# Performance work log

Measured on AMD Instinct MI355X. Metric: run time of the kernel, lower is better.

Reference implementation:

```python
import jax, jax.numpy as jnp
import numpy as np

THETA = 10000.0
NUM_HEADS = 16


def _rope(x, positions):
    # x: [B, H, S, Dk] (fp32), positions: [B, S] int
    d_k = x.shape[-1]
    k = jnp.arange(0, d_k, 2, dtype=jnp.float32)
    freqs = THETA ** (-k / d_k)                      # [Dk/2]
    angles = positions[..., None].astype(jnp.float32) * freqs  # [B, S, Dk/2]
    cos = jnp.cos(angles)[:, None, :, :]             # [B, 1, S, Dk/2]
    sin = jnp.sin(angles)[:, None, :, :]
    xr = x.reshape(*x.shape[:-1], d_k // 2, 2)
    x_even, x_odd = xr[..., 0], xr[..., 1]
    rot_even = x_even * cos - x_odd * sin
    rot_odd = x_even * sin + x_odd * cos
    out = jnp.stack([rot_even, rot_odd], axis=-1)
    return out.reshape(x.shape)


def setup_inputs() -> dict:
    key = jax.random.key(0)
    ks = jax.random.split(key, 6)
    B, S, D = 2, 2048, 1024
    std = (2.0 / (D + D)) ** 0.5
    x = jax.random.normal(ks[0], (B, S, D), dtype=jnp.float32)
    Wq = jax.random.normal(ks[1], (D, D), dtype=jnp.float32) * std
    Wk = jax.random.normal(ks[2], (D, D), dtype=jnp.float32) * std
    Wv = jax.random.normal(ks[3], (D, D), dtype=jnp.float32) * std
    Wo = jax.random.normal(ks[4], (D, D), dtype=jnp.float32) * std
    token_positions = jnp.broadcast_to(jnp.arange(S, dtype=jnp.int32), (B, S))
    return {"x": x, "Wq": Wq, "Wk": Wk, "Wv": Wv, "Wo": Wo,
            "token_positions": token_positions}


def reference(x, Wq, Wk, Wv, Wo, token_positions):
    B, S, D = x.shape
    H = NUM_HEADS
    Dk = D // H
    # QKV projections (no bias): y = x @ W.T
    def proj(W):
        return (x @ W.T).reshape(B, S, H, Dk).transpose(0, 2, 1, 3)  # [B,H,S,Dk]
    Q, K, V = proj(Wq), proj(Wk), proj(Wv)
    Q = _rope(Q, token_positions)
    K = _rope(K, token_positions)
    scale = 1.0 / jnp.sqrt(jnp.float32(Dk))
    scores = jnp.einsum('bhqd,bhkd->bhqk', Q, K) * scale  # [B,H,S,S]
    causal = jnp.tril(jnp.ones((S, S), dtype=bool))
    scores = jnp.where(causal, scores, -jnp.inf)
    attn = jax.nn.softmax(scores.astype(jnp.float32), axis=-1)
    out = jnp.einsum('bhqk,bhkd->bhqd', attn, V)          # [B,H,S,Dk]
    out = out.transpose(0, 2, 1, 3).reshape(B, S, D)
    return out @ Wo.T
```

## Files before the change

kernel.cpp:

```cpp
#include <hip/hip_runtime.h>
#include <math.h>

#define D_MODEL 1024
#define NHEADS 16
#define DK 64
#define SEQ 2048
#define BATCH 2
#define MROWS (BATCH * SEQ)

typedef __attribute__((ext_vector_type(8))) short bfrag8;
typedef __attribute__((ext_vector_type(4))) float f32x4;
typedef unsigned short u16;
typedef __attribute__((ext_vector_type(8))) u16 u16x8;
typedef __attribute__((ext_vector_type(4))) u16 u16x4;

#define GLOBAL_AS(p) ((const __attribute__((address_space(1))) void*)(p))
#define LDS_AS(p)    ((__attribute__((address_space(3))) void*)(p))

#define RAW_BARRIER()  __asm__ volatile("s_barrier" ::: "memory")
#define WAIT_VM4()     __asm__ volatile("s_waitcnt vmcnt(4)" ::: "memory")
#define WAIT_VM0()     __asm__ volatile("s_waitcnt vmcnt(0)" ::: "memory")

__device__ inline u16 f2bf(float f) {
  union { float f; unsigned u; } c; c.f = f;
  unsigned r = c.u + 0x7FFF + ((c.u >> 16) & 1);
  return (u16)(r >> 16);
}

__device__ inline unsigned pack_bf2(float lo, float hi) {
  return __builtin_amdgcn_perm(__float_as_uint(hi), __float_as_uint(lo), 0x07060302);
}

struct CvtPtrs { const float* src[5]; };

__global__ __launch_bounds__(256)
void convert_and_tab(CvtPtrs p, u16* __restrict__ dst,
                     const int* __restrict__ pos, float2* __restrict__ tab) {
  const int bi = blockIdx.x;
  if (bi < 8192) {
    size_t base = ((size_t)bi * 256 + threadIdx.x) * 4;
    const size_t XSZ = (size_t)MROWS * D_MODEL;
    const float* s; size_t off;
    if (base < XSZ) { s = p.src[0]; off = base; }
    else {
      size_t j = base - XSZ;
      s = p.src[1 + (int)(j >> 20)];
      off = j & ((1u << 20) - 1);
    }
    float4 v = *(const float4*)(s + off);
    u16 o[4] = { f2bf(v.x), f2bf(v.y), f2bf(v.z), f2bf(v.w) };
    *(u16x4*)(dst + base) = *(u16x4*)o;
  } else {
    int idx = (bi - 8192) * 256 + threadIdx.x;
    int i = idx & 31, bs = idx >> 5;
    float pp = (float)pos[bs];
    float freq = expf(-(float)i * 0.2878231366242558f);
    float sn, cs;
    sincosf(pp * freq, &sn, &cs);
    tab[idx] = make_float2(cs, sn);
  }
}

__device__ inline void gemm_core(const u16* __restrict__ A, const u16* __restrict__ B,
                                 int m0, int n0, u16* As, u16* Bs,
                                 f32x4 acc[4][4]) {
  const int tid = threadIdx.x;
  const int w = tid >> 6, lane = tid & 63;
  const int l15 = lane & 15, quad = lane >> 4;
  const int wm = w >> 1, wn = w & 1;
  const int srow = tid >> 2;
  const int scol = (tid & 3) * 8;

  #pragma unroll
  for (int mi = 0; mi < 4; ++mi)
    #pragma unroll
    for (int ni = 0; ni < 4; ++ni) acc[mi][ni] = (f32x4)0.f;

  for (int k0 = 0; k0 < D_MODEL; k0 += 32) {
    __syncthreads();
    #pragma unroll
    for (int i = 0; i < 2; ++i) {
      const u16* ga = A + (size_t)((i * 64 + srow) + m0) * D_MODEL + k0 + scol;
      const u16* gb = B + (size_t)((i * 64 + srow) + n0) * D_MODEL + k0 + scol;
      __builtin_amdgcn_global_load_lds(GLOBAL_AS(ga), LDS_AS(&As[(i * 64 + w * 16) * 32]), 16, 0, 0);
      __builtin_amdgcn_global_load_lds(GLOBAL_AS(gb), LDS_AS(&Bs[(i * 64 + w * 16) * 32]), 16, 0, 0);
    }
    __syncthreads();

    bfrag8 af[4], bfr[4];
    #pragma unroll
    for (int i = 0; i < 4; ++i) {
      af[i]  = *(const bfrag8*)&As[(wm * 64 + i * 16 + l15) * 32 + quad * 8];
      bfr[i] = *(const bfrag8*)&Bs[(wn * 64 + i * 16 + l15) * 32 + quad * 8];
    }
    #pragma unroll
    for (int mi = 0; mi < 4; ++mi)
      #pragma unroll
      for (int ni = 0; ni < 4; ++ni)
        acc[mi][ni] = __builtin_amdgcn_mfma_f32_16x16x32_bf16(af[mi], bfr[ni], acc[mi][ni], 0, 0, 0);
  }
}

struct QKVArgs { const u16* A[3]; const u16* B[3]; u16* dst[3]; const float2* tab; };

__global__ __launch_bounds__(256)
void gemm_qkv_fused(QKVArgs p) {
  __shared__ u16 As[128 * 32];
  __shared__ u16 Bs[128 * 32];
  const int z = blockIdx.z;
  const int bi = blockIdx.x;
  int m0, n0;
  if (z < 2) { m0 = (bi & 7) * 128; n0 = (bi >> 3) * 128; }
  else       { m0 = (bi >> 3) * 128; n0 = (bi & 7) * 128; }
  f32x4 acc[4][4];
  gemm_core(p.A[z], p.B[z], m0, n0, As, Bs, acc);

  const int tid = threadIdx.x;
  const int w = tid >> 6, lane = tid & 63;
  const int l15 = lane & 15, quad = lane >> 4;
  const int wm = w >> 1, wn = w & 1;
  u16* dst = p.dst[z];

  if (z < 2) {
    const int head = (m0 + wm * 64) >> 6;
    const float scale = (z == 0) ? 0.125f * 1.4426950408889634f : 1.0f;
    #pragma unroll
    for (int ni = 0; ni < 4; ++ni) {
      int sg = n0 + wn * 64 + ni * 16 + l15;
      int b = sg >> 11;
      int s = sg & (SEQ - 1);
      size_t ho = ((size_t)(b * NHEADS + head)) * SEQ * DK;
      #pragma unroll
      for (int mi = 0; mi < 4; ++mi) {
        float4 t = *(const float4*)&p.tab[(size_t)sg * 32 + mi * 8 + quad * 2];
        float e0 = acc[mi][ni][0], o0 = acc[mi][ni][1];
        float e1 = acc[mi][ni][2], o1 = acc[mi][ni][3];
        u16x4 ov = { f2bf((e0 * t.x - o0 * t.y) * scale),
                     f2bf((e0 * t.y + o0 * t.x) * scale),
                     f2bf((e1 * t.z - o1 * t.w) * scale),
                     f2bf((e1 * t.w + o1 * t.z) * scale) };
        *(u16x4*)&dst[ho + (size_t)s * DK + mi * 16 + quad * 4] = ov;
      }
    }
  } else {
    const int b = m0 >> 11;
    const int head = (n0 >> 6) + wn;
    const size_t ho = ((size_t)(b * NHEADS + head)) * SEQ * DK;
    const int row_base = m0 + wm * 64;
    #pragma unroll
    for (int mi = 0; mi < 4; ++mi)
      #pragma unroll
      for (int ni = 0; ni < 4; ++ni) {
        int d = ni * 16 + l15;
        int sb = (row_base + mi * 16 + quad * 4) & (SEQ - 1);
        u16 o[4];
        #pragma unroll
        for (int r = 0; r < 4; ++r) o[r] = f2bf(acc[mi][ni][r]);
        *(u16x4*)&dst[ho + (size_t)d * SEQ + sb] = *(u16x4*)o;
      }
  }
}

__global__ __launch_bounds__(256)
void gemm_out_bf16(const u16* __restrict__ A, const u16* __restrict__ B,
                   float* __restrict__ C) {
  __shared__ u16 As[128 * 32];
  __shared__ u16 Bs[64 * 32];
  const int m0 = blockIdx.y * 128, n0 = blockIdx.x * 64;
  const int tid = threadIdx.x;
  const int w = tid >> 6, lane = tid & 63;
  const int l15 = lane & 15, quad = lane >> 4;
  const int wm = w >> 1, wn = w & 1;
  const int lrow = lane >> 2;
  const int lcol = (lane & 3) * 8;

  f32x4 acc[4][2];
  #pragma unroll
  for (int mi = 0; mi < 4; ++mi)
    #pragma unroll
    for (int ni = 0; ni < 2; ++ni) acc[mi][ni] = (f32x4)0.f;

  for (int k0 = 0; k0 < D_MODEL; k0 += 32) {
    __syncthreads();
    #pragma unroll
    for (int i = 0; i < 2; ++i) {
      int row = (i * 4 + w) * 16 + lrow;
      const u16* ga = A + (size_t)(m0 + row) * D_MODEL + k0 + lcol;
      __builtin_amdgcn_global_load_lds(GLOBAL_AS(ga), LDS_AS(&As[(i * 4 + w) * 16 * 32]), 16, 0, 0);
    }
    {
      int row = w * 16 + lrow;
      const u16* gb = B + (size_t)(n0 + row) * D_MODEL + k0 + lcol;
      __builtin_amdgcn_global_load_lds(GLOBAL_AS(gb), LDS_AS(&Bs[w * 16 * 32]), 16, 0, 0);
    }
    __syncthreads();

    bfrag8 af[4], bfr[2];
    #pragma unroll
    for (int i = 0; i < 4; ++i)
      af[i] = *(const bfrag8*)&As[(wm * 64 + i * 16 + l15) * 32 + quad * 8];
    #pragma unroll
    for (int i = 0; i < 2; ++i)
      bfr[i] = *(const bfrag8*)&Bs[(wn * 32 + i * 16 + l15) * 32 + quad * 8];
    #pragma unroll
    for (int mi = 0; mi < 4; ++mi)
      #pragma unroll
      for (int ni = 0; ni < 2; ++ni)
        acc[mi][ni] = __builtin_amdgcn_mfma_f32_16x16x32_bf16(af[mi], bfr[ni], acc[mi][ni], 0, 0, 0);
  }

  #pragma unroll
  for (int mi = 0; mi < 4; ++mi)
    #pragma unroll
    for (int ni = 0; ni < 2; ++ni)
      #pragma unroll
      for (int r = 0; r < 4; ++r) {
        int row = m0 + wm * 64 + mi * 16 + quad * 4 + r;
        int col = n0 + wn * 32 + ni * 16 + l15;
        C[(size_t)row * D_MODEL + col] = acc[mi][ni][r];
      }
}

__global__ __launch_bounds__(256, 4)
void attn_mfma(const u16* __restrict__ Qbf, const u16* __restrict__ Kbf,
               const u16* __restrict__ Vtb, u16* __restrict__ obb) {
  __shared__ u16 Ks[2][64 * 64];
  __shared__ u16 Vt[2][64 * 64];

  const int tid = threadIdx.x;
  const int w = tid >> 6, lane = tid & 63;
  const int l15 = lane & 15, quad = lane >> 4;

  const int bid = blockIdx.x;
  const int hb = bid & 31;
  const int g  = bid >> 5;
  const int tt = (g & 7) | ((g & 16) >> 1);
  const int qt = (g & 8) ? (31 - tt) : tt;
  const int b = hb >> 4, h = hb & 15;
  const size_t ho = (size_t)hb * SEQ * DK;
  const int qrow_base = qt * 64 + w * 16;

  bfrag8 qf[2];
  #pragma unroll
  for (int hh = 0; hh < 2; ++hh)
    qf[hh] = *(const bfrag8*)&Qbf[ho + (size_t)(qrow_base + l15) * DK + hh * 32 + quad * 8];

  f32x4 oacc[4];
  float l_ = 0.f;
  #pragma unroll
  for (int n0 = 0; n0 < 4; ++n0) oacc[n0] = (f32x4)0.f;

  const int srow = w * 8 + (lane >> 3);
  const int scc = ((lane & 7) ^ (srow & 7)) * 8;

  const int adr0 = (((quad & 1) << 5) + l15) << 2;
  const int adr1 = adr0 + 64;

  #define STAGE(T, BUF) do {                                                         \
    int j0_ = (T) * 64;                                                              \
    _Pragma("unroll")                                                                \
    for (int r_ = 0; r_ < 2; ++r_) {                                                 \
      int row_ = r_ * 32 + srow;                                                     \
      __builtin_amdgcn_global_load_lds(GLOBAL_AS(Kbf + ho + (size_t)(j0_ + row_) * DK + scc), \
                                       LDS_AS(&Ks[BUF][(r_ * 32 + w * 8) * 64]), 16, 0, 0);   \
      __builtin_amdgcn_global_load_lds(GLOBAL_AS(Vtb + ho + (size_t)row_ * SEQ + j0_ + scc),  \
                                       LDS_AS(&Vt[BUF][(r_ * 32 + w * 8) * 64]), 16, 0, 0);   \
    }                                                                                \
  } while (0)

  const int ntiles = qt + 1;
  STAGE(0, 0);

  for (int t = 0; t < ntiles; ++t) {
    const int j0 = t * 64;
    const int buf = t & 1;
    RAW_BARRIER();
    if (t + 1 < ntiles) {
      STAGE(t + 1, buf ^ 1);
      WAIT_VM4();
    } else {
      WAIT_VM0();
    }
    RAW_BARRIER();

    f32x4 sc[4];
    const int sw = l15 & 7;
    #pragma unroll
    for (int st = 0; st < 4; ++st) {
      int key = st * 16 + l15;
      bfrag8 kf0 = *(const bfrag8*)&Ks[buf][key * 64 + ((quad ^ sw) * 8)];
      bfrag8 kf1 = *(const bfrag8*)&Ks[buf][key * 64 + (((4 + quad) ^ sw) * 8)];
      sc[st] = __builtin_amdgcn_mfma_f32_16x16x32_bf16(kf0, qf[0], (f32x4)0.f, 0, 0, 0);
      sc[st] = __builtin_amdgcn_mfma_f32_16x16x32_bf16(kf1, qf[1], sc[st], 0, 0, 0);
    }

    if (j0 + 63 > qrow_base) {
      #pragma unroll
      for (int st = 0; st < 4; ++st)
        #pragma unroll
        for (int r = 0; r < 4; ++r) {
          int key = j0 + st * 16 + quad * 4 + r;
          if (key > qrow_base + l15) sc[st][r] = -60.f;
        }
    }

    unsigned pk[4][2];
    float rs = 0.f;
    #pragma unroll
    for (int st = 0; st < 4; ++st) {
      float p0 = __builtin_amdgcn_exp2f(fminf(sc[st][0], 60.f));
      float p1 = __builtin_amdgcn_exp2f(fminf(sc[st][1], 60.f));
      float p2 = __builtin_amdgcn_exp2f(fminf(sc[st][2], 60.f));
      float p3 = __builtin_amdgcn_exp2f(fminf(sc[st][3], 60.f));
      rs += (p0 + p1) + (p2 + p3);
      pk[st][0] = pack_bf2(p0, p1);
      pk[st][1] = pack_bf2(p2, p3);
    }
    l_ += rs;

    union PU { bfrag8 f; int i[4]; } u0, u1;
    #pragma unroll
    for (int j = 0; j < 4; ++j) {
      const int adr = (j & 2) ? adr1 : adr0;
      int lo0 = __builtin_amdgcn_ds_bpermute(adr, (int)pk[0][j & 1]);
      int hi0 = __builtin_amdgcn_ds_bpermute(adr, (int)pk[1][j & 1]);
      int lo1 = __builtin_amdgcn_ds_bpermute(adr, (int)pk[2][j & 1]);
      int hi1 = __builtin_amdgcn_ds_bpermute(adr, (int)pk[3][j & 1]);
      u0.i[j] = (quad & 2) ? hi0 : lo0;
      u1.i[j] = (quad & 2) ? hi1 : lo1;
    }
    bfrag8 pf[2] = { u0.f, u1.f };

    #pragma unroll
    for (int n0 = 0; n0 < 4; ++n0) {
      #pragma unroll
      for (int kc = 0; kc < 2; ++kc) {
        bfrag8 vf = *(const bfrag8*)&Vt[buf][(n0 * 16 + l15) * 64 + (((kc * 4 + quad) ^ sw) * 8)];
        oacc[n0] = __builtin_amdgcn_mfma_f32_16x16x32_bf16(vf, pf[kc], oacc[n0], 0, 0, 0);
      }
    }
  }
  #undef STAGE

  float l = l_;
  l += __shfl_xor(l, 16);
  l += __shfl_xor(l, 32);
  float inv = 1.f / l;
  int q = qrow_base + l15;
  #pragma unroll
  for (int n0 = 0; n0 < 4; ++n0) {
    u16x4 ov = { f2bf(oacc[n0][0] * inv), f2bf(oacc[n0][1] * inv),
                 f2bf(oacc[n0][2] * inv), f2bf(oacc[n0][3] * inv) };
    *(u16x4*)&obb[(size_t)(b * SEQ + q) * D_MODEL + h * DK + n0 * 16 + quad * 4] = ov;
  }
}

extern "C" void kernel_launch(void* const* d_in, const int* in_sizes, int n_in,
                              void* d_out, int out_size, void* d_ws, size_t ws_size,
                              hipStream_t stream) {
  const float* x  = (const float*)d_in[0];
  const float* Wq = (const float*)d_in[1];
  const float* Wk = (const float*)d_in[2];
  const float* Wv = (const float*)d_in[3];
  const float* Wo = (const float*)d_in[4];
  const int* pos  = (const int*)d_in[5];

  const size_t XSZ = (size_t)MROWS * D_MODEL;
  const size_t WSZ = (size_t)D_MODEL * D_MODEL;

  u16* bfb = (u16*)d_ws;
  u16* xb  = bfb;
  u16* wqb = xb  + XSZ;
  u16* wkb = wqb + WSZ;
  u16* wvb = wkb + WSZ;
  u16* wob = wvb + WSZ;
  u16* Qbf = wob + WSZ;
  u16* Kbf = Qbf + XSZ;
  u16* Vtb = Kbf + XSZ;
  u16* obb = Vtb + XSZ;
  float2* tab = (float2*)(obb + XSZ);

  CvtPtrs cp; cp.src[0] = x; cp.src[1] = Wq; cp.src[2] = Wk; cp.src[3] = Wv; cp.src[4] = Wo;
  convert_and_tab<<<8192 + 512, 256, 0, stream>>>(cp, xb, pos, tab);

  QKVArgs qp;
  qp.A[0] = wqb; qp.A[1] = wkb; qp.A[2] = xb;
  qp.B[0] = xb;  qp.B[1] = xb;  qp.B[2] = wvb;
  qp.dst[0] = Qbf; qp.dst[1] = Kbf; qp.dst[2] = Vtb;
  qp.tab = tab;
  gemm_qkv_fused<<<dim3(256, 1, 3), 256, 0, stream>>>(qp);

  attn_mfma<<<dim3(1024), 256, 0, stream>>>(Qbf, Kbf, Vtb, obb);

  gemm_out_bf16<<<dim3(D_MODEL / 64, MROWS / 128), 256, 0, stream>>>(obb, wob, (float*)d_out);
}
```

Baseline: 182.7 us.

## Triple-buffer QKV GEMM LDS tiles with async prefetch two stages ahead

Replaces the single-buffered k-loop in the shared GEMM core with a three-stage ring of LDS buffers. Each iteration prefetches tile t+2 with global_load_lds and waits on a vmcnt count only until tile t has landed. The per-tile `__syncthreads` pairs become raw barriers. The aim is to hide global-memory latency behind MFMA work, at the cost of three times the LDS in the QKV kernel, which may lower occupancy. Any other kernel that calls `gemm_core` with smaller LDS arrays would need the same resize.

```diff
diff --git a/kernel.cpp b/kernel.cpp
--- a/kernel.cpp
+++ b/kernel.cpp
@@ -18,6 +18,7 @@
 #define LDS_AS(p)    ((__attribute__((address_space(3))) void*)(p))
 
 #define RAW_BARRIER()  __asm__ volatile("s_barrier" ::: "memory")
+#define WAIT_VM8()     __asm__ volatile("s_waitcnt vmcnt(8)" ::: "memory")
 #define WAIT_VM4()     __asm__ volatile("s_waitcnt vmcnt(4)" ::: "memory")
 #define WAIT_VM0()     __asm__ volatile("s_waitcnt vmcnt(0)" ::: "memory")
 
@@ -76,37 +77,59 @@
     #pragma unroll
     for (int ni = 0; ni < 4; ++ni) acc[mi][ni] = (f32x4)0.f;
 
-  for (int k0 = 0; k0 < D_MODEL; k0 += 32) {
-    __syncthreads();
-    #pragma unroll
-    for (int i = 0; i < 2; ++i) {
-      const u16* ga = A + (size_t)((i * 64 + srow) + m0) * D_MODEL + k0 + scol;
-      const u16* gb = B + (size_t)((i * 64 + srow) + n0) * D_MODEL + k0 + scol;
-      __builtin_amdgcn_global_load_lds(GLOBAL_AS(ga), LDS_AS(&As[(i * 64 + w * 16) * 32]), 16, 0, 0);
-      __builtin_amdgcn_global_load_lds(GLOBAL_AS(gb), LDS_AS(&Bs[(i * 64 + w * 16) * 32]), 16, 0, 0);
-    }
-    __syncthreads();
+  #define GSTAGE(T, BUF) do {                                                        \
+    _Pragma("unroll")                                                                \
+    for (int i_ = 0; i_ < 2; ++i_) {                                                 \
+      const u16* ga_ = A + (size_t)((i_ * 64 + srow) + m0) * D_MODEL + (T) * 32 + scol; \
+      const u16* gb_ = B + (size_t)((i_ * 64 + srow) + n0) * D_MODEL + (T) * 32 + scol; \
+      __builtin_amdgcn_global_load_lds(GLOBAL_AS(ga_),                               \
+          LDS_AS(&As[(BUF) * 4096 + (i_ * 64 + w * 16) * 32]), 16, 0, 0);            \
+      __builtin_amdgcn_global_load_lds(GLOBAL_AS(gb_),                               \
+          LDS_AS(&Bs[(BUF) * 4096 + (i_ * 64 + w * 16) * 32]), 16, 0, 0);            \
+    }                                                                                \
+  } while (0)
+
+  const int NT = D_MODEL / 32;
+  GSTAGE(0, 0);
+  GSTAGE(1, 1);
+  int sbuf = 2;
+  int cbuf = 0;
+  for (int t = 0; t < NT; ++t) {
+    RAW_BARRIER();
+    if (t + 2 < NT) {
+      GSTAGE(t + 2, sbuf);
+      WAIT_VM8();
+    } else if (t + 1 < NT) {
+      WAIT_VM4();
+    } else {
+      WAIT_VM0();
+    }
+    RAW_BARRIER();
 
     bfrag8 af[4], bfr[4];
     #pragma unroll
     for (int i = 0; i < 4; ++i) {
-      af[i]  = *(const bfrag8*)&As[(wm * 64 + i * 16 + l15) * 32 + quad * 8];
-      bfr[i] = *(const bfrag8*)&Bs[(wn * 64 + i * 16 + l15) * 32 + quad * 8];
+      af[i]  = *(const bfrag8*)&As[cbuf * 4096 + (wm * 64 + i * 16 + l15) * 32 + quad * 8];
+      bfr[i] = *(const bfrag8*)&Bs[cbuf * 4096 + (wn * 64 + i * 16 + l15) * 32 + quad * 8];
     }
     #pragma unroll
     for (int mi = 0; mi < 4; ++mi)
       #pragma unroll
       for (int ni = 0; ni < 4; ++ni)
         acc[mi][ni] = __builtin_amdgcn_mfma_f32_16x16x32_bf16(af[mi], bfr[ni], acc[mi][ni], 0, 0, 0);
-  }
+
+    sbuf = cbuf;
+    cbuf = (cbuf == 2) ? 0 : cbuf + 1;
+  }
+  #undef GSTAGE
 }
 
 struct QKVArgs { const u16* A[3]; const u16* B[3]; u16* dst[3]; const float2* tab; };
 
 __global__ __launch_bounds__(256)
 void gemm_qkv_fused(QKVArgs p) {
-  __shared__ u16 As[128 * 32];
-  __shared__ u16 Bs[128 * 32];
+  __shared__ u16 As[3 * 128 * 32];
+  __shared__ u16 Bs[3 * 128 * 32];
   const int z = blockIdx.z;
   const int bi = blockIdx.x;
   int m0, n0;
```

After: 180.9 us. About the same (-1.0%).
